# Kernel tuning notes

Measured on AMD Instinct MI355X. Metric: run time of the kernel, lower is better.

## Reference

```python
import jax, jax.numpy as jnp
import numpy as np

NLIG = 16384
NPROT = 131072
N = NLIG + NPROT
E = 2097152
B = 256
H = 64


def setup_inputs() -> dict:
    key = jax.random.key(0)
    ks = jax.random.split(key, 40)
    i = iter(range(40))

    def nrm(shape, scale=0.1):
        return (jax.random.normal(ks[next(i)], shape, jnp.float32) * scale)

    inp = {
        'lig_pos': nrm((NLIG, 3), 1.0),
        'lig_feat': nrm((NLIG, 15), 1.0),
        'prot_pos': nrm((NPROT, 3), 1.0),
        'prot_feat': nrm((NPROT, 8), 1.0),
        't': jax.random.uniform(ks[next(i)], (B,), jnp.float32) * 1000.0,
        'lig_batch': jnp.sort(jax.random.randint(ks[next(i)], (NLIG,), 0, B)),
        'prot_batch': jnp.sort(jax.random.randint(ks[next(i)], (NPROT,), 0, B)),
        'edge_index': jax.random.randint(ks[next(i)], (2, E), 0, N),
        'W_lig': nrm((15, H)), 'b_lig': nrm((H,)),
        'W_prot': nrm((8, H)), 'b_prot': nrm((H,)),
        'Wt1': nrm((H, H)), 'bt1': nrm((H,)),
        'Wt2': nrm((H, H)), 'bt2': nrm((H,)),
        'Wrel1': nrm((H, H)), 'brel1': nrm((H,)), 'Wroot1': nrm((H, H)),
        'Wrel2': nrm((H, H)), 'brel2': nrm((H,)), 'Wroot2': nrm((H, H)),
        'Wrel3': nrm((H, H)), 'brel3': nrm((H,)), 'Wroot3': nrm((H, H)),
        'Wro1': nrm((H, H)), 'bro1': nrm((H,)),
        'Wro2': nrm((H, 1)), 'bro2': nrm((1,)),
    }
    return inp


def _time_embedding(t, dim):
    half = dim // 2
    freqs = jnp.exp(jnp.arange(half, dtype=jnp.float32) * (-np.log(10000.0) / (half - 1)))
    e = t[:, None] * freqs[None, :]  # [B, half]
    return jnp.concatenate([jnp.sin(e), jnp.cos(e)], axis=-1)  # [B, dim]


def _silu(x):
    return x * jax.nn.sigmoid(x)


def _graph_conv(x, src, dst, Wrel, brel, Wroot):
    # PyG GraphConv (aggr='add'): lin_rel(sum_j x_j) + lin_root(x)
    agg = jax.ops.segment_sum(x[src], dst, num_segments=N)  # [N, H]
    return agg @ Wrel + brel + x @ Wroot


def reference(lig_pos, lig_feat, prot_pos, prot_feat, t, lig_batch, prot_batch,
              edge_index, W_lig, b_lig, W_prot, b_prot, Wt1, bt1, Wt2, bt2,
              Wrel1, brel1, Wroot1, Wrel2, brel2, Wroot2, Wrel3, brel3, Wroot3,
              Wro1, bro1, Wro2, bro2):
    t_emb = _time_embedding(t, H)                      # [B, H]
    t_emb = _silu(t_emb @ Wt1 + bt1) @ Wt2 + bt2       # time_mlp
    x_lig = lig_feat @ W_lig + b_lig + t_emb[lig_batch]
    x_prot = prot_feat @ W_prot + b_prot
    x = jnp.concatenate([x_lig, x_prot], axis=0)       # [N, H]

    src, dst = edge_index[0], edge_index[1]
    x = _graph_conv(x, src, dst, Wrel1, brel1, Wroot1)
    x = _graph_conv(x, src, dst, Wrel2, brel2, Wroot2)
    x = _graph_conv(x, src, dst, Wrel3, brel3, Wroot3)

    # global_mean_pool over ligand nodes
    lig_x = x[:NLIG]
    sums = jax.ops.segment_sum(lig_x, lig_batch, num_segments=B)  # [B, H]
    cnt = jax.ops.segment_sum(jnp.ones((NLIG,), jnp.float32), lig_batch, num_segments=B)
    pooled = sums / jnp.maximum(cnt, 1.0)[:, None]

    return _silu(pooled @ Wro1 + bro1) @ Wro2 + bro2   # [B, 1]
```

## Files before the change

### kernel.cpp

```cpp
#include <hip/hip_runtime.h>
#include <math.h>

#define NLIG 16384
#define NPROT 131072
#define NTOT (NLIG + NPROT)
#define NEDGE 2097152
#define NB 256
#define H 64
#define NBUCK 576
#define BSHIFT 8
#define BCAP 4608
#define NPW 24

typedef short v4s __attribute__((ext_vector_type(4)));
typedef float v4f __attribute__((ext_vector_type(4)));

__device__ __forceinline__ unsigned short f2bf(float f) {
    unsigned int u = __float_as_uint(f);
    u += 0x7fff + ((u >> 16) & 1);
    return (unsigned short)(u >> 16);
}
__device__ __forceinline__ float bf2f(unsigned short s) {
    return __uint_as_float(((unsigned int)s) << 16);
}
__device__ __forceinline__ float bflo(unsigned int u) {
    return __uint_as_float(u << 16);
}
__device__ __forceinline__ float bfhi(unsigned int u) {
    return __uint_as_float(u & 0xffff0000u);
}

__global__ __launch_bounds__(1024) void megaA_kernel(const int* __restrict__ edge_index,
                                                     unsigned int* __restrict__ bcursor,
                                                     unsigned int* __restrict__ bucketed,
                                                     const float* __restrict__ t,
                                                     const float* __restrict__ Wt1, const float* __restrict__ bt1,
                                                     const float* __restrict__ Wt2, const float* __restrict__ bt2,
                                                     const float* __restrict__ W0, const float* __restrict__ W1,
                                                     const float* __restrict__ W2, const float* __restrict__ W3,
                                                     const float* __restrict__ W4, const float* __restrict__ W5,
                                                     unsigned short* __restrict__ wbuf,
                                                     float* __restrict__ t_emb) {
    __shared__ unsigned int lh[NBUCK];
    __shared__ unsigned int lcur[NBUCK];
    __shared__ unsigned int gb[NBUCK];
    __shared__ float emb_s[16][H];
    __shared__ float h1_s[16][H];
    int b = blockIdx.x, tid = threadIdx.x;
    if (b < 256) {
        for (int i = tid; i < NBUCK; i += 1024) lh[i] = 0;
        __syncthreads();
        int e0 = b * 8192;
        int src[8], dst[8];
        #pragma unroll
        for (int k = 0; k < 8; k++) {
            src[k] = edge_index[e0 + k * 1024 + tid];
            dst[k] = edge_index[NEDGE + e0 + k * 1024 + tid];
            atomicAdd(&lh[dst[k] >> BSHIFT], 1);
        }
        __syncthreads();
        if (tid < NBUCK) {
            gb[tid] = atomicAdd(&bcursor[tid], lh[tid]);
            lcur[tid] = 0;
        }
        __syncthreads();
        #pragma unroll
        for (int k = 0; k < 8; k++) {
            int bb = dst[k] >> BSHIFT;
            unsigned int r = atomicAdd(&lcur[bb], 1);
            unsigned int slot = gb[bb] + r;
            if (slot < BCAP)
                bucketed[bb * BCAP + slot] =
                    (unsigned int)src[k] | ((unsigned int)(dst[k] & 255) << 18);
        }
    } else if (b < 280) {
        const float* Ws[6] = {W0, W1, W2, W3, W4, W5};
        int tglob = (b - 256) * 1024 + tid;
        int m = tglob >> 12, tt = tglob & 4095;
        int f = tt >> 8, l = (tt >> 2) & 63, i = tt & 3;
        int kt = f >> 2, ct = f & 3;
        int row = 16 * kt + 4 * (l >> 4) + i;
        int col = 16 * ct + (l & 15);
        wbuf[m * 4096 + tt] = f2bf(Ws[m][row * H + col]);
    } else {
        int w = tid >> 6, h = tid & 63;
        int bb = (b - 280) * 16 + w;
        float tv = t[bb];
        int i = h & 31;
        float freq = expf((float)i * (-9.2103403719761836f / 31.0f));
        float e = tv * freq;
        emb_s[w][h] = (h < 32) ? sinf(e) : cosf(e);
        __syncthreads();
        float acc = bt1[h];
        #pragma unroll 8
        for (int k = 0; k < H; k++) acc += emb_s[w][k] * Wt1[k * H + h];
        float sig = 1.0f / (1.0f + expf(-acc));
        h1_s[w][h] = acc * sig;
        __syncthreads();
        float acc2 = bt2[h];
        #pragma unroll 8
        for (int k = 0; k < H; k++) acc2 += h1_s[w][k] * Wt2[k * H + h];
        t_emb[bb * H + h] = acc2;
    }
}

__global__ __launch_bounds__(1024) void megaB_kernel(const unsigned int* __restrict__ bucketed,
                                                     const unsigned int* __restrict__ bcursor,
                                                     int* __restrict__ off,
                                                     int* __restrict__ ends,
                                                     int* __restrict__ csr_src,
                                                     const float* __restrict__ lig_feat,
                                                     const float* __restrict__ prot_feat,
                                                     const int* __restrict__ lig_batch,
                                                     const float* __restrict__ t_emb,
                                                     const float* __restrict__ W_lig,
                                                     const float* __restrict__ b_lig,
                                                     const float* __restrict__ W_prot,
                                                     const float* __restrict__ b_prot,
                                                     unsigned int* __restrict__ xb) {
    __shared__ unsigned int stage[BCAP];
    __shared__ unsigned int csr_l[BCAP];
    __shared__ unsigned int lh[256];
    __shared__ unsigned int sc[256];
    __shared__ unsigned int lcur[256];
    int b = blockIdx.x, tid = threadIdx.x;
    if (b < NBUCK) {
        unsigned int base = (unsigned int)b * BCAP;
        int cnt = (int)bcursor[b];
        if (cnt > BCAP) cnt = BCAP;
        if (tid < 256) lh[tid] = 0;
        __syncthreads();
        for (int i = tid; i < cnt; i += 1024) {
            unsigned int v = bucketed[base + i];
            stage[i] = v;
            atomicAdd(&lh[v >> 18], 1);
        }
        __syncthreads();
        if (tid < 256) sc[tid] = lh[tid];
        __syncthreads();
        #pragma unroll
        for (int d = 1; d < 256; d <<= 1) {
            unsigned int v = (tid < 256 && tid >= (unsigned)d) ? sc[tid - d] : 0;
            __syncthreads();
            if (tid < 256) sc[tid] += v;
            __syncthreads();
        }
        if (tid < 256) {
            unsigned int excl = sc[tid] - lh[tid];
            lcur[tid] = excl;
            off[b * 256 + tid]  = (int)(base + excl);
            ends[b * 256 + tid] = (int)(base + excl + lh[tid]);
        }
        __syncthreads();
        for (int i = tid; i < cnt; i += 1024) {
            unsigned int v = stage[i];
            unsigned int p = atomicAdd(&lcur[v >> 18], 1);
            csr_l[p] = v & 0x3ffffu;
        }
        __syncthreads();
        for (int i = tid; i < cnt; i += 1024)
            csr_src[base + i] = (int)csr_l[i];
    } else {
        int node = (b - NBUCK) * 16 + (tid >> 6);
        int h = tid & 63;
        float acc;
        if (node < NLIG) {
            int bb = lig_batch[node];
            acc = b_lig[h] + t_emb[bb * H + h];
            #pragma unroll
            for (int k = 0; k < 15; k++)
                acc += lig_feat[node * 15 + k] * W_lig[k * H + h];
        } else {
            int p = node - NLIG;
            acc = b_prot[h];
            #pragma unroll
            for (int k = 0; k < 8; k++)
                acc += prot_feat[p * 8 + k] * W_prot[k * H + h];
        }
        float e0 = __shfl(acc, 2 * (h & 31));
        float e1 = __shfl(acc, 2 * (h & 31) + 1);
        if (h < 32)
            xb[node * 32 + h] = (unsigned int)f2bf(e0) | ((unsigned int)f2bf(e1) << 16);
    }
}

#define ACC8(u)                                   \
    do {                                          \
        a0 += bflo((u).x); a1 += bfhi((u).x);     \
        a2 += bflo((u).y); a3 += bfhi((u).y);     \
        a4 += bflo((u).z); a5 += bfhi((u).z);     \
        a6 += bflo((u).w); a7 += bfhi((u).w);     \
    } while (0)

#define DO_GROUP(BEG, DEG, IDFIRST, AGGROW)                                     \
    {                                                                           \
        int idcur = (IDFIRST);                                                  \
        float a0 = 0.f, a1 = 0.f, a2 = 0.f, a3 = 0.f;                           \
        float a4 = 0.f, a5 = 0.f, a6 = 0.f, a7 = 0.f;                           \
        for (int jb = 0; jb < (DEG); jb += 8) {                                 \
            int idnxt = (jb + 8 + q < (DEG)) ? csr[(BEG) + jb + 8 + q] : -1;    \
            int n0 = __shfl(idcur, s * 8 + 0);                                  \
            int n1 = __shfl(idcur, s * 8 + 1);                                  \
            int n2 = __shfl(idcur, s * 8 + 2);                                  \
            int n3 = __shfl(idcur, s * 8 + 3);                                  \
            int n4 = __shfl(idcur, s * 8 + 4);                                  \
            int n5 = __shfl(idcur, s * 8 + 5);                                  \
            int n6 = __shfl(idcur, s * 8 + 6);                                  \
            int n7 = __shfl(idcur, s * 8 + 7);                                  \
            int c1 = (n1 >= 0) ? n1 : n0;                                       \
            int c2 = (n2 >= 0) ? n2 : n0;                                       \
            int c3 = (n3 >= 0) ? n3 : n0;                                       \
            int c4 = (n4 >= 0) ? n4 : n0;                                       \
            int c5 = (n5 >= 0) ? n5 : n0;                                       \
            int c6 = (n6 >= 0) ? n6 : n0;                                       \
            int c7 = (n7 >= 0) ? n7 : n0;                                       \
            uint4 u0 = *(const uint4*)&xb[n0 * 32 + q * 4];                     \
            uint4 u1 = *(const uint4*)&xb[c1 * 32 + q * 4];                     \
            uint4 u2 = *(const uint4*)&xb[c2 * 32 + q * 4];                     \
            uint4 u3 = *(const uint4*)&xb[c3 * 32 + q * 4];                     \
            uint4 u4 = *(const uint4*)&xb[c4 * 32 + q * 4];                     \
            uint4 u5 = *(const uint4*)&xb[c5 * 32 + q * 4];                     \
            uint4 u6 = *(const uint4*)&xb[c6 * 32 + q * 4];                     \
            uint4 u7 = *(const uint4*)&xb[c7 * 32 + q * 4];                     \
            if (n1 < 0) { u1.x = u1.y = u1.z = u1.w = 0; }                      \
            if (n2 < 0) { u2.x = u2.y = u2.z = u2.w = 0; }                      \
            if (n3 < 0) { u3.x = u3.y = u3.z = u3.w = 0; }                      \
            if (n4 < 0) { u4.x = u4.y = u4.z = u4.w = 0; }                      \
            if (n5 < 0) { u5.x = u5.y = u5.z = u5.w = 0; }                      \
            if (n6 < 0) { u6.x = u6.y = u6.z = u6.w = 0; }                      \
            if (n7 < 0) { u7.x = u7.y = u7.z = u7.w = 0; }                      \
            ACC8(u0); ACC8(u1); ACC8(u2); ACC8(u3);                             \
            ACC8(u4); ACC8(u5); ACC8(u6); ACC8(u7);                             \
            idcur = idnxt;                                                      \
        }                                                                       \
        unsigned int p0 = (unsigned int)f2bf(a0) | ((unsigned int)f2bf(a1) << 16); \
        unsigned int p1 = (unsigned int)f2bf(a2) | ((unsigned int)f2bf(a3) << 16); \
        unsigned int p2 = (unsigned int)f2bf(a4) | ((unsigned int)f2bf(a5) << 16); \
        unsigned int p3 = (unsigned int)f2bf(a6) | ((unsigned int)f2bf(a7) << 16); \
        *(uint4*)&agg_s[(AGGROW) * 72 + q * 8] = make_uint4(p0, p1, p2, p3);    \
    }

__global__ __launch_bounds__(512, 6) void conv_kernel(const int* __restrict__ off,
                                                      const int* __restrict__ ends,
                                                      const int* __restrict__ csr,
                                                      const unsigned int* __restrict__ xb,
                                                      const unsigned short* __restrict__ wbuf,
                                                      const float* __restrict__ brel,
                                                      unsigned int* __restrict__ xob) {
    __shared__ unsigned int wlds[4096];
    __shared__ unsigned short agg_s[8 * NPW * 72];
    const int tid = threadIdx.x;
    const int w = tid >> 6, l = tid & 63;
    const unsigned int* wsrc = (const unsigned int*)wbuf;
    #pragma unroll
    for (int i = 0; i < 8; i++) wlds[i * 512 + tid] = wsrc[i * 512 + tid];

    const int s = l >> 3, q = l & 7;
    const int lrow = l & 15, g16 = l >> 4, g4 = 4 * (l >> 4);
    const int gwid = blockIdx.x * 8 + w;
    const int node0w = gwid * NPW;

    int bvv = (l < NPW) ? off[node0w + l] : 0;
    int evv = (l < NPW) ? ends[node0w + l] : 0;

    int b0 = __shfl(bvv, s),      d0 = __shfl(evv, s) - b0;
    int b1 = __shfl(bvv, 8 + s),  d1 = __shfl(evv, 8 + s) - b1;
    int b2 = __shfl(bvv, 16 + s), d2 = __shfl(evv, 16 + s) - b2;
    int id0 = (q < d0) ? csr[b0 + q] : -1;
    int id1 = (q < d1) ? csr[b1 + q] : -1;
    int id2 = (q < d2) ? csr[b2 + q] : -1;

    __syncthreads();

    float bv[4];
    #pragma unroll
    for (int ct = 0; ct < 4; ct++) bv[ct] = brel[ct * 16 + lrow];

    DO_GROUP(b0, d0, id0, w * NPW + s)
    DO_GROUP(b1, d1, id1, w * NPW + 8 + s)
    DO_GROUP(b2, d2, id2, w * NPW + 16 + s)

    __builtin_amdgcn_wave_barrier();

    v4s ax[4];
    #pragma unroll
    for (int kt = 0; kt < 4; kt++)
        ax[kt] = *(const v4s*)&xb[(node0w + lrow) * 32 + kt * 8 + g16 * 2];
    v4f acc[4];
    #pragma unroll
    for (int ct = 0; ct < 4; ct++) acc[ct] = (v4f){0.f, 0.f, 0.f, 0.f};
    #pragma unroll
    for (int kt = 0; kt < 4; kt++) {
        v4s a_agg = *(const v4s*)&agg_s[(w * NPW + lrow) * 72 + kt * 16 + g4];
        #pragma unroll
        for (int ct = 0; ct < 4; ct++) {
            int f = kt * 4 + ct;
            v4s wr = *(const v4s*)&wlds[f * 128 + l * 2];
            v4s wo = *(const v4s*)&wlds[2048 + f * 128 + l * 2];
            acc[ct] = __builtin_amdgcn_mfma_f32_16x16x16bf16_1k(a_agg, wr, acc[ct], 0, 0, 0);
            acc[ct] = __builtin_amdgcn_mfma_f32_16x16x16bf16_1k(ax[kt], wo, acc[ct], 0, 0, 0);
        }
    }
    const int r2row = 16 + (l & 7);
    v4s ax2[4];
    #pragma unroll
    for (int kt = 0; kt < 4; kt++)
        ax2[kt] = *(const v4s*)&xb[(node0w + r2row) * 32 + kt * 8 + g16 * 2];
    v4f acc2[4];
    #pragma unroll
    for (int ct = 0; ct < 4; ct++) acc2[ct] = (v4f){0.f, 0.f, 0.f, 0.f};
    #pragma unroll
    for (int kt = 0; kt < 4; kt++) {
        v4s a_agg2 = *(const v4s*)&agg_s[(w * NPW + r2row) * 72 + kt * 16 + g4];
        #pragma unroll
        for (int ct = 0; ct < 4; ct++) {
            int f = kt * 4 + ct;
            v4s wr = *(const v4s*)&wlds[f * 128 + l * 2];
            v4s wo = *(const v4s*)&wlds[2048 + f * 128 + l * 2];
            acc2[ct] = __builtin_amdgcn_mfma_f32_16x16x16bf16_1k(a_agg2, wr, acc2[ct], 0, 0, 0);
            acc2[ct] = __builtin_amdgcn_mfma_f32_16x16x16bf16_1k(ax2[kt], wo, acc2[ct], 0, 0, 0);
        }
    }
    __builtin_amdgcn_wave_barrier();

    #pragma unroll
    for (int ct = 0; ct < 4; ct++) {
        #pragma unroll
        for (int r = 0; r < 4; r++)
            agg_s[(w * NPW + g4 + r) * 72 + ct * 16 + lrow] = f2bf(acc[ct][r] + bv[ct]);
    }
    if (g16 < 2) {
        #pragma unroll
        for (int ct = 0; ct < 4; ct++) {
            #pragma unroll
            for (int r = 0; r < 4; r++)
                agg_s[(w * NPW + 16 + g4 + r) * 72 + ct * 16 + lrow] =
                    f2bf(acc2[ct][r] + bv[ct]);
        }
    }
    __builtin_amdgcn_wave_barrier();

    {
        int row = l >> 2, qq = l & 3;
        const unsigned int* srcp = (const unsigned int*)&agg_s[(w * NPW + row) * 72 + qq * 16];
        uint4 v0 = *(const uint4*)(srcp);
        uint4 v1 = *(const uint4*)(srcp + 4);
        *(uint4*)&xob[(node0w + row) * 32 + qq * 8] = v0;
        *(uint4*)&xob[(node0w + row) * 32 + qq * 8 + 4] = v1;
    }
    {
        int row = 16 + (l >> 3), qq = l & 7;
        *(uint4*)&xob[(node0w + row) * 32 + qq * 4] =
            *(const uint4*)&agg_s[(w * NPW + row) * 72 + qq * 8];
    }
}

__global__ __launch_bounds__(512, 6) void conv_lig_kernel(const int* __restrict__ off,
                                                          const int* __restrict__ ends,
                                                          const int* __restrict__ csr,
                                                          const unsigned int* __restrict__ xb,
                                                          const unsigned short* __restrict__ wbuf,
                                                          const float* __restrict__ brel,
                                                          const int* __restrict__ lig_batch,
                                                          float* __restrict__ pooled,
                                                          float* __restrict__ cnt) {
    __shared__ unsigned int wlds[4096];
    __shared__ unsigned short agg_s[8 * 8 * 72];
    const int tid = threadIdx.x;
    const int w = tid >> 6, l = tid & 63;
    const unsigned int* wsrc = (const unsigned int*)wbuf;
    #pragma unroll
    for (int i = 0; i < 8; i++) wlds[i * 512 + tid] = wsrc[i * 512 + tid];

    const int s = l >> 3, q = l & 7;
    const int lrow = l & 15, g16 = l >> 4, g4 = 4 * (l >> 4);
    const int gwid = blockIdx.x * 8 + w;
    const int node0w = gwid * 8;

    int bvv = (l < 8) ? off[node0w + l] : 0;
    int evv = (l < 8) ? ends[node0w + l] : 0;
    int b0 = __shfl(bvv, s), d0 = __shfl(evv, s) - b0;
    int id0 = (q < d0) ? csr[b0 + q] : -1;

    __syncthreads();

    float bv[4];
    #pragma unroll
    for (int ct = 0; ct < 4; ct++) bv[ct] = brel[ct * 16 + lrow];

    DO_GROUP(b0, d0, id0, w * 8 + s)

    __builtin_amdgcn_wave_barrier();

    const int arow = lrow & 7;
    v4s ax[4];
    #pragma unroll
    for (int kt = 0; kt < 4; kt++)
        ax[kt] = *(const v4s*)&xb[(node0w + arow) * 32 + kt * 8 + g16 * 2];
    v4f acc[4];
    #pragma unroll
    for (int ct = 0; ct < 4; ct++) acc[ct] = (v4f){0.f, 0.f, 0.f, 0.f};
    #pragma unroll
    for (int kt = 0; kt < 4; kt++) {
        v4s a_agg = *(const v4s*)&agg_s[(w * 8 + arow) * 72 + kt * 16 + g4];
        #pragma unroll
        for (int ct = 0; ct < 4; ct++) {
            int f = kt * 4 + ct;
            v4s wr = *(const v4s*)&wlds[f * 128 + l * 2];
            v4s wo = *(const v4s*)&wlds[2048 + f * 128 + l * 2];
            acc[ct] = __builtin_amdgcn_mfma_f32_16x16x16bf16_1k(a_agg, wr, acc[ct], 0, 0, 0);
            acc[ct] = __builtin_amdgcn_mfma_f32_16x16x16bf16_1k(ax[kt], wo, acc[ct], 0, 0, 0);
        }
    }

    if (g16 < 2) {
        #pragma unroll
        for (int r = 0; r < 4; r++) {
            int node = node0w + g4 + r;
            int bb = lig_batch[node];
            #pragma unroll
            for (int ct = 0; ct < 4; ct++)
                unsafeAtomicAdd(&pooled[bb * H + ct * 16 + lrow], acc[ct][r] + bv[ct]);
            if (lrow == 0) unsafeAtomicAdd(&cnt[bb], 1.0f);
        }
    }
}

__global__ void readout_kernel(const float* __restrict__ pooled, const float* __restrict__ cnt,
                               const float* __restrict__ Wro1, const float* __restrict__ bro1,
                               const float* __restrict__ Wro2, const float* __restrict__ bro2,
                               float* __restrict__ out) {
    __shared__ float pm[4][H];
    int w = threadIdx.x >> 6;
    int h = threadIdx.x & 63;
    int b = blockIdx.x * 4 + w;
    float c = fmaxf(cnt[b], 1.0f);
    pm[w][h] = pooled[b * H + h] / c;
    __syncthreads();
    float acc = bro1[h];
    #pragma unroll 8
    for (int k = 0; k < H; k++) acc += pm[w][k] * Wro1[k * H + h];
    float sig = 1.0f / (1.0f + expf(-acc));
    float s = acc * sig;
    float r = s * Wro2[h];
    #pragma unroll
    for (int off = 32; off; off >>= 1) r += __shfl_down(r, off);
    if (h == 0) out[b] = r + bro2[0];
}

extern "C" void kernel_launch(void* const* d_in, const int* in_sizes, int n_in,
                              void* d_out, int out_size, void* d_ws, size_t ws_size,
                              hipStream_t stream) {
    const float* lig_feat  = (const float*)d_in[1];
    const float* prot_feat = (const float*)d_in[3];
    const float* t         = (const float*)d_in[4];
    const int*   lig_batch = (const int*)d_in[5];
    const int*   edge_index= (const int*)d_in[7];
    const float* W_lig  = (const float*)d_in[8];
    const float* b_lig  = (const float*)d_in[9];
    const float* W_prot = (const float*)d_in[10];
    const float* b_prot = (const float*)d_in[11];
    const float* Wt1 = (const float*)d_in[12];
    const float* bt1 = (const float*)d_in[13];
    const float* Wt2 = (const float*)d_in[14];
    const float* bt2 = (const float*)d_in[15];
    const float* Wrel[3]  = {(const float*)d_in[16], (const float*)d_in[19], (const float*)d_in[22]};
    const float* brel[3]  = {(const float*)d_in[17], (const float*)d_in[20], (const float*)d_in[23]};
    const float* Wroot[3] = {(const float*)d_in[18], (const float*)d_in[21], (const float*)d_in[24]};
    const float* Wro1 = (const float*)d_in[25];
    const float* bro1 = (const float*)d_in[26];
    const float* Wro2 = (const float*)d_in[27];
    const float* bro2 = (const float*)d_in[28];
    float* out = (float*)d_out;

    char* ws = (char*)d_ws;
    int*            off_a   = (int*)(ws);
    int*            ends_a  = (int*)(ws + 655360);
    unsigned int*   bcursor = (unsigned int*)(ws + 1310720);
    float*          pooled  = (float*)(ws + 1313024);
    float*          cnt     = (float*)(ws + 1378560);
    float*          t_emb   = (float*)(ws + 1380352);
    unsigned short* wbuf    = (unsigned short*)(ws + 1572864);
    int*            csr_src = (int*)(ws + 2097152);
    unsigned int*   bucketed= (unsigned int*)(ws + 14680064);
    unsigned int*   xb0     = (unsigned int*)(ws + 27262976);
    unsigned int*   xb1     = (unsigned int*)(ws + 46137344);

    hipMemsetAsync(bcursor, 0, 68864, stream);

    megaA_kernel<<<296, 1024, 0, stream>>>(edge_index, bcursor, bucketed,
                                           t, Wt1, bt1, Wt2, bt2,
                                           Wrel[0], Wroot[0], Wrel[1], Wroot[1], Wrel[2], Wroot[2],
                                           wbuf, t_emb);

    megaB_kernel<<<NBUCK + NTOT / 16, 1024, 0, stream>>>(bucketed, bcursor,
                                                         off_a, ends_a, csr_src,
                                                         lig_feat, prot_feat, lig_batch, t_emb,
                                                         W_lig, b_lig, W_prot, b_prot, xb0);

    conv_kernel<<<768, 512, 0, stream>>>(off_a, ends_a, csr_src, xb0,
                                         wbuf, brel[0], xb1);
    conv_kernel<<<768, 512, 0, stream>>>(off_a, ends_a, csr_src, xb1,
                                         wbuf + 8192, brel[1], xb0);
    conv_lig_kernel<<<NLIG / 64, 512, 0, stream>>>(off_a, ends_a, csr_src, xb0,
                                                   wbuf + 16384, brel[2], lig_batch,
                                                   pooled, cnt);

    readout_kernel<<<NB / 4, 256, 0, stream>>>(pooled, cnt, Wro1, bro1, Wro2, bro2, out);
}
```

Baseline: 213.7 us.

## Restructure preprocessing kernels: move bucket fill next to node init, fold memset into prep

Reorganizes the preprocessing pipeline into three kernels. A small prep kernel computes the time MLP, packs the weights and zeroes the bucket cursors, replacing the separate memset. The edge bucketing now runs alongside node-feature initialization, with 128 blocks of 16K edges each that reload edge indices instead of keeping them in registers. CSR construction becomes its own kernel. This removes the memset launch and changes which work overlaps, but it adds a launch and splits the CSR pass from the node-init blocks it previously ran beside.

```diff
diff --git a/kernel.cpp b/kernel.cpp
--- a/kernel.cpp
+++ b/kernel.cpp
@@ -30,61 +30,30 @@
     return __uint_as_float(u & 0xffff0000u);
 }
 
-__global__ __launch_bounds__(1024) void megaA_kernel(const int* __restrict__ edge_index,
-                                                     unsigned int* __restrict__ bcursor,
-                                                     unsigned int* __restrict__ bucketed,
-                                                     const float* __restrict__ t,
+__global__ __launch_bounds__(1024) void prep2_kernel(const float* __restrict__ t,
                                                      const float* __restrict__ Wt1, const float* __restrict__ bt1,
                                                      const float* __restrict__ Wt2, const float* __restrict__ bt2,
                                                      const float* __restrict__ W0, const float* __restrict__ W1,
                                                      const float* __restrict__ W2, const float* __restrict__ W3,
                                                      const float* __restrict__ W4, const float* __restrict__ W5,
                                                      unsigned short* __restrict__ wbuf,
-                                                     float* __restrict__ t_emb) {
-    __shared__ unsigned int lh[NBUCK];
-    __shared__ unsigned int lcur[NBUCK];
-    __shared__ unsigned int gb[NBUCK];
-    __shared__ float emb_s[16][H];
-    __shared__ float h1_s[16][H];
+                                                     float* __restrict__ t_emb,
+                                                     unsigned int* __restrict__ zero_region) {
     int b = blockIdx.x, tid = threadIdx.x;
-    if (b < 256) {
-        for (int i = tid; i < NBUCK; i += 1024) lh[i] = 0;
-        __syncthreads();
-        int e0 = b * 8192;
-        int src[8], dst[8];
-        #pragma unroll
-        for (int k = 0; k < 8; k++) {
-            src[k] = edge_index[e0 + k * 1024 + tid];
-            dst[k] = edge_index[NEDGE + e0 + k * 1024 + tid];
-            atomicAdd(&lh[dst[k] >> BSHIFT], 1);
-        }
-        __syncthreads();
-        if (tid < NBUCK) {
-            gb[tid] = atomicAdd(&bcursor[tid], lh[tid]);
-            lcur[tid] = 0;
-        }
-        __syncthreads();
-        #pragma unroll
-        for (int k = 0; k < 8; k++) {
-            int bb = dst[k] >> BSHIFT;
-            unsigned int r = atomicAdd(&lcur[bb], 1);
-            unsigned int slot = gb[bb] + r;
-            if (slot < BCAP)
-                bucketed[bb * BCAP + slot] =
-                    (unsigned int)src[k] | ((unsigned int)(dst[k] & 255) << 18);
-        }
-    } else if (b < 280) {
+    if (b < 24) {
         const float* Ws[6] = {W0, W1, W2, W3, W4, W5};
-        int tglob = (b - 256) * 1024 + tid;
+        int tglob = b * 1024 + tid;
         int m = tglob >> 12, tt = tglob & 4095;
         int f = tt >> 8, l = (tt >> 2) & 63, i = tt & 3;
         int kt = f >> 2, ct = f & 3;
         int row = 16 * kt + 4 * (l >> 4) + i;
         int col = 16 * ct + (l & 15);
         wbuf[m * 4096 + tt] = f2bf(Ws[m][row * H + col]);
-    } else {
+    } else if (b < 40) {
+        __shared__ float emb_s[16][H];
+        __shared__ float h1_s[16][H];
         int w = tid >> 6, h = tid & 63;
-        int bb = (b - 280) * 16 + w;
+        int bb = (b - 24) * 16 + w;
         float tv = t[bb];
         int i = h & 31;
         float freq = expf((float)i * (-9.2103403719761836f / 31.0f));
@@ -101,67 +70,55 @@
         #pragma unroll 8
         for (int k = 0; k < H; k++) acc2 += h1_s[w][k] * Wt2[k * H + h];
         t_emb[bb * H + h] = acc2;
-    }
-}
-
-__global__ __launch_bounds__(1024) void megaB_kernel(const unsigned int* __restrict__ bucketed,
-                                                     const unsigned int* __restrict__ bcursor,
-                                                     int* __restrict__ off,
-                                                     int* __restrict__ ends,
-                                                     int* __restrict__ csr_src,
-                                                     const float* __restrict__ lig_feat,
-                                                     const float* __restrict__ prot_feat,
-                                                     const int* __restrict__ lig_batch,
-                                                     const float* __restrict__ t_emb,
-                                                     const float* __restrict__ W_lig,
-                                                     const float* __restrict__ b_lig,
-                                                     const float* __restrict__ W_prot,
-                                                     const float* __restrict__ b_prot,
-                                                     unsigned int* __restrict__ xb) {
-    __shared__ unsigned int stage[BCAP];
-    __shared__ unsigned int csr_l[BCAP];
-    __shared__ unsigned int lh[256];
-    __shared__ unsigned int sc[256];
-    __shared__ unsigned int lcur[256];
+    } else {
+        for (int i = tid; i < 17216; i += 1024) zero_region[i] = 0;
+    }
+}
+
+__global__ __launch_bounds__(1024) void fill_init_kernel(const int* __restrict__ edge_index,
+                                                         unsigned int* __restrict__ bcursor,
+                                                         unsigned int* __restrict__ bucketed,
+                                                         const float* __restrict__ lig_feat,
+                                                         const float* __restrict__ prot_feat,
+                                                         const int* __restrict__ lig_batch,
+                                                         const float* __restrict__ t_emb,
+                                                         const float* __restrict__ W_lig,
+                                                         const float* __restrict__ b_lig,
+                                                         const float* __restrict__ W_prot,
+                                                         const float* __restrict__ b_prot,
+                                                         unsigned int* __restrict__ xb) {
     int b = blockIdx.x, tid = threadIdx.x;
-    if (b < NBUCK) {
-        unsigned int base = (unsigned int)b * BCAP;
-        int cnt = (int)bcursor[b];
-        if (cnt > BCAP) cnt = BCAP;
-        if (tid < 256) lh[tid] = 0;
-        __syncthreads();
-        for (int i = tid; i < cnt; i += 1024) {
-            unsigned int v = bucketed[base + i];
-            stage[i] = v;
-            atomicAdd(&lh[v >> 18], 1);
-        }
-        __syncthreads();
-        if (tid < 256) sc[tid] = lh[tid];
-        __syncthreads();
-        #pragma unroll
-        for (int d = 1; d < 256; d <<= 1) {
-            unsigned int v = (tid < 256 && tid >= (unsigned)d) ? sc[tid - d] : 0;
-            __syncthreads();
-            if (tid < 256) sc[tid] += v;
-            __syncthreads();
-        }
-        if (tid < 256) {
-            unsigned int excl = sc[tid] - lh[tid];
-            lcur[tid] = excl;
-            off[b * 256 + tid]  = (int)(base + excl);
-            ends[b * 256 + tid] = (int)(base + excl + lh[tid]);
-        }
-        __syncthreads();
-        for (int i = tid; i < cnt; i += 1024) {
-            unsigned int v = stage[i];
-            unsigned int p = atomicAdd(&lcur[v >> 18], 1);
-            csr_l[p] = v & 0x3ffffu;
-        }
-        __syncthreads();
-        for (int i = tid; i < cnt; i += 1024)
-            csr_src[base + i] = (int)csr_l[i];
+    if (b < 128) {
+        __shared__ unsigned int lh[NBUCK];
+        __shared__ unsigned int lcur[NBUCK];
+        __shared__ unsigned int gb[NBUCK];
+        for (int i = tid; i < NBUCK; i += 1024) lh[i] = 0;
+        __syncthreads();
+        int e0 = b * 16384;
+        #pragma unroll
+        for (int k = 0; k < 16; k++) {
+            int d = edge_index[NEDGE + e0 + k * 1024 + tid];
+            atomicAdd(&lh[d >> BSHIFT], 1);
+        }
+        __syncthreads();
+        if (tid < NBUCK) {
+            gb[tid] = atomicAdd(&bcursor[tid], lh[tid]);
+            lcur[tid] = 0;
+        }
+        __syncthreads();
+        #pragma unroll
+        for (int k = 0; k < 16; k++) {
+            int srcv = edge_index[e0 + k * 1024 + tid];
+            int dstv = edge_index[NEDGE + e0 + k * 1024 + tid];
+            int bb = dstv >> BSHIFT;
+            unsigned int r = atomicAdd(&lcur[bb], 1);
+            unsigned int slot = gb[bb] + r;
+            if (slot < BCAP)
+                bucketed[bb * BCAP + slot] =
+                    (unsigned int)srcv | ((unsigned int)(dstv & 255) << 18);
+        }
     } else {
-        int node = (b - NBUCK) * 16 + (tid >> 6);
+        int node = (b - 128) * 16 + (tid >> 6);
         int h = tid & 63;
         float acc;
         if (node < NLIG) {
@@ -182,6 +139,54 @@
         if (h < 32)
             xb[node * 32 + h] = (unsigned int)f2bf(e0) | ((unsigned int)f2bf(e1) << 16);
     }
+}
+
+__global__ __launch_bounds__(1024) void bucket_csr_kernel(const unsigned int* __restrict__ bucketed,
+                                                          const unsigned int* __restrict__ bcursor,
+                                                          int* __restrict__ off,
+                                                          int* __restrict__ ends,
+                                                          int* __restrict__ csr_src) {
+    __shared__ unsigned int stage[BCAP];
+    __shared__ unsigned int csr_l[BCAP];
+    __shared__ unsigned int lh[256];
+    __shared__ unsigned int sc[256];
+    __shared__ unsigned int lcur[256];
+    int b = blockIdx.x, tid = threadIdx.x;
+    unsigned int base = (unsigned int)b * BCAP;
+    int cnt = (int)bcursor[b];
+    if (cnt > BCAP) cnt = BCAP;
+    if (tid < 256) lh[tid] = 0;
+    __syncthreads();
+    for (int i = tid; i < cnt; i += 1024) {
+        unsigned int v = bucketed[base + i];
+        stage[i] = v;
+        atomicAdd(&lh[v >> 18], 1);
+    }
+    __syncthreads();
+    if (tid < 256) sc[tid] = lh[tid];
+    __syncthreads();
+    #pragma unroll
+    for (int d = 1; d < 256; d <<= 1) {
+        unsigned int v = (tid < 256 && tid >= (unsigned)d) ? sc[tid - d] : 0;
+        __syncthreads();
+        if (tid < 256) sc[tid] += v;
+        __syncthreads();
+    }
+    if (tid < 256) {
+        unsigned int excl = sc[tid] - lh[tid];
+        lcur[tid] = excl;
+        off[b * 256 + tid]  = (int)(base + excl);
+        ends[b * 256 + tid] = (int)(base + excl + lh[tid]);
+    }
+    __syncthreads();
+    for (int i = tid; i < cnt; i += 1024) {
+        unsigned int v = stage[i];
+        unsigned int p = atomicAdd(&lcur[v >> 18], 1);
+        csr_l[p] = v & 0x3ffffu;
+    }
+    __syncthreads();
+    for (int i = tid; i < cnt; i += 1024)
+        csr_src[base + i] = (int)csr_l[i];
 }
 
 #define ACC8(u)                                   \
@@ -486,17 +491,15 @@
     unsigned int*   xb0     = (unsigned int*)(ws + 27262976);
     unsigned int*   xb1     = (unsigned int*)(ws + 46137344);
 
-    hipMemsetAsync(bcursor, 0, 68864, stream);
-
-    megaA_kernel<<<296, 1024, 0, stream>>>(edge_index, bcursor, bucketed,
-                                           t, Wt1, bt1, Wt2, bt2,
-                                           Wrel[0], Wroot[0], Wrel[1], Wroot[1], Wrel[2], Wroot[2],
-                                           wbuf, t_emb);
-
-    megaB_kernel<<<NBUCK + NTOT / 16, 1024, 0, stream>>>(bucketed, bcursor,
-                                                         off_a, ends_a, csr_src,
-                                                         lig_feat, prot_feat, lig_batch, t_emb,
-                                                         W_lig, b_lig, W_prot, b_prot, xb0);
+    prep2_kernel<<<41, 1024, 0, stream>>>(t, Wt1, bt1, Wt2, bt2,
+                                          Wrel[0], Wroot[0], Wrel[1], Wroot[1], Wrel[2], Wroot[2],
+                                          wbuf, t_emb, bcursor);
+
+    fill_init_kernel<<<128 + NTOT / 16, 1024, 0, stream>>>(edge_index, bcursor, bucketed,
+                                                           lig_feat, prot_feat, lig_batch, t_emb,
+                                                           W_lig, b_lig, W_prot, b_prot, xb0);
+
+    bucket_csr_kernel<<<NBUCK, 1024, 0, stream>>>(bucketed, bcursor, off_a, ends_a, csr_src);
 
     conv_kernel<<<768, 512, 0, stream>>>(off_a, ends_a, csr_src, xb0,
                                          wbuf, brel[0], xb1);
```

Result: faster. 208.2 us (-2.6%).
